# Performance work log

Hardware: AMD Instinct MI355X
Metric: run time of the kernel (lower is better)

Reference implementation:

```python
import jax, jax.numpy as jnp
import numpy as np

B, F, V, D, H = 16384, 45, 10000, 256, 32


def setup_inputs() -> dict:
    key = jax.random.key(0)
    ks = jax.random.split(key, 6)
    src = jax.random.randint(ks[0], (B, F), 0, V, dtype=jnp.int64 if jax.config.jax_enable_x64 else jnp.int32)
    tables = jax.random.normal(ks[1], (F, V, D), dtype=jnp.float32) * 0.02
    W1 = jax.random.normal(ks[2], (D, H), dtype=jnp.float32) * 0.05
    b1 = jax.random.normal(ks[3], (H,), dtype=jnp.float32) * 0.05
    W2 = jax.random.normal(ks[4], (H, 1), dtype=jnp.float32) * 0.05
    b2 = jax.random.normal(ks[5], (1,), dtype=jnp.float32) * 0.05
    return {"src": src, "tables": tables, "W1": W1, "b1": b1, "W2": W2, "b2": b2}


def reference(src, tables, W1, b1, W2, b2):
    # Fused multi-table gather: emb[b, f] = tables[f, src[b, f]]  -> [B, F, D]
    feat_idx = jnp.arange(F)[None, :]            # [1, F]
    emb = tables[feat_idx, src]                  # [B, F, D]
    # Small MLP applied per feature position, then sum over features.
    h = jnp.einsum('bfd,dh->bfh', emb, W1) + b1  # [B, F, 32]
    out = jnp.einsum('bfh,ho->bfo', h, W2) + b2  # [B, F, 1]
    return jnp.sum(out, axis=1)                  # [B, 1]
```

## Files before the change

### kernel.cpp

```cpp
#include <hip/hip_runtime.h>


#define BN 16384
#define FN 45
#define VN 10000
#define DN 256
#define HN 32

__global__ void prep_w_kernel(const float* __restrict__ W1,
                              const float* __restrict__ b1,
                              const float* __restrict__ W2,
                              const float* __restrict__ b2,
                              float* __restrict__ w_out,
                              float* __restrict__ c_out) {
    int d = threadIdx.x;
    float s = 0.f;
#pragma unroll
    for (int h = 0; h < HN; ++h) s += W1[d * HN + h] * W2[h];
    w_out[d] = s;
    if (d == 0) {
        float cc = 0.f;
#pragma unroll
        for (int h = 0; h < HN; ++h) cc += b1[h] * W2[h];
        c_out[0] = cc + b2[0];
    }
}

__global__ __launch_bounds__(256, 8)
void row_dot_kernel(const float* __restrict__ tables,
                    const float* __restrict__ w,
                    float* __restrict__ t,
                    int R) {
    const int lane = threadIdx.x & 63;
    const int wave_in_block = threadIdx.x >> 6;
    const int waves_per_block = blockDim.x >> 6;
    const int nwaves = gridDim.x * waves_per_block;
    int wave = blockIdx.x * waves_per_block + wave_in_block;

    const float4 wv = reinterpret_cast<const float4*>(w)[lane];

    for (int r = wave; r < R; r += nwaves) {
        const float4 v =
            reinterpret_cast<const float4*>(tables + (size_t)r * DN)[lane];
        float s = v.x * wv.x + v.y * wv.y + v.z * wv.z + v.w * wv.w;
#pragma unroll
        for (int m = 1; m < 64; m <<= 1) s += __shfl_xor(s, m);
        if (lane == 0) t[r] = s;
    }
}

__global__ __launch_bounds__(256)
void gather_sum_kernel(const int* __restrict__ src,
                       const float* __restrict__ t,
                       const float* __restrict__ c,
                       float* __restrict__ out) {
    const int lane = threadIdx.x & 63;
    const int wave = blockIdx.x * (blockDim.x >> 6) + (threadIdx.x >> 6);
    if (wave >= BN) return;

    float s = 0.f;
    if (lane < FN) {
        const int idx = src[wave * FN + lane];
        s = t[lane * VN + idx];
    }
#pragma unroll
    for (int m = 1; m < 64; m <<= 1) s += __shfl_xor(s, m);
    if (lane == 0) out[wave] = s + (float)FN * c[0];
}

extern "C" void kernel_launch(void* const* d_in, const int* in_sizes, int n_in,
                              void* d_out, int out_size, void* d_ws, size_t ws_size,
                              hipStream_t stream) {
    const int* src = (const int*)d_in[0];
    const float* tables = (const float*)d_in[1];
    const float* W1 = (const float*)d_in[2];
    const float* b1 = (const float*)d_in[3];
    const float* W2 = (const float*)d_in[4];
    const float* b2 = (const float*)d_in[5];
    float* out = (float*)d_out;

    float* ws = (float*)d_ws;
    float* w = ws;
    float* c = ws + 256;
    float* t = ws + 512;
    const int R = FN * VN;

    prep_w_kernel<<<1, 256, 0, stream>>>(W1, b1, W2, b2, w, c);

    row_dot_kernel<<<2048, 256, 0, stream>>>(tables, w, t, R);

    gather_sum_kernel<<<4096, 256, 0, stream>>>(src, t, c, out);
}
```

Measured before the change: 598.6 us.

## Fuse into cooperative kernel and skip table rows never referenced by src

```diff
diff --git a/kernel.cpp b/kernel.cpp
--- a/kernel.cpp
+++ b/kernel.cpp
@@ -1,4 +1,7 @@
 #include <hip/hip_runtime.h>
+#include <hip/hip_cooperative_groups.h>
+
+namespace cg = cooperative_groups;
 
 
 #define BN 16384
@@ -6,66 +9,77 @@
 #define VN 10000
 #define DN 256
 #define HN 32
+#define RN (FN * VN)
+#define NBLK 1024
+#define NTHR 256
+#define NWAVE (NBLK * 4)
+#define NTHREADS (NBLK * NTHR)
 
-__global__ void prep_w_kernel(const float* __restrict__ W1,
-                              const float* __restrict__ b1,
-                              const float* __restrict__ W2,
-                              const float* __restrict__ b2,
-                              float* __restrict__ w_out,
-                              float* __restrict__ c_out) {
-    int d = threadIdx.x;
-    float s = 0.f;
+__global__ __launch_bounds__(NTHR, 4)
+void fused_kernel(const int* __restrict__ src,
+                  const float* __restrict__ tables,
+                  const float* __restrict__ W1,
+                  const float* __restrict__ b1,
+                  const float* __restrict__ W2,
+                  const float* __restrict__ b2,
+                  float* __restrict__ out,
+                  float* __restrict__ t,
+                  unsigned char* __restrict__ flags) {
+    cg::grid_group grid = cg::this_grid();
+    const int tid = threadIdx.x;
+    const int lane = tid & 63;
+    const int wid = tid >> 6;
+    const int gwave = blockIdx.x * 4 + wid;
+    const int gtid = blockIdx.x * NTHR + tid;
+
+    __shared__ __align__(16) float w_s[DN];
+    __shared__ float c_s;
+
+    {
+        float s = 0.f;
 #pragma unroll
-    for (int h = 0; h < HN; ++h) s += W1[d * HN + h] * W2[h];
-    w_out[d] = s;
-    if (d == 0) {
-        float cc = 0.f;
+        for (int h = 0; h < HN; ++h) s += W1[tid * HN + h] * W2[h];
+        w_s[tid] = s;
+        if (tid == 0) {
+            float cc = 0.f;
 #pragma unroll
-        for (int h = 0; h < HN; ++h) cc += b1[h] * W2[h];
-        c_out[0] = cc + b2[0];
+            for (int h = 0; h < HN; ++h) cc += b1[h] * W2[h];
+            c_s = (float)FN * (cc + b2[0]);
+        }
     }
-}
+    {
+        unsigned int* fw = reinterpret_cast<unsigned int*>(flags);
+        for (int i = gtid; i < RN / 4; i += NTHREADS) fw[i] = 0u;
+    }
+    grid.sync();
 
-__global__ __launch_bounds__(256, 8)
-void row_dot_kernel(const float* __restrict__ tables,
-                    const float* __restrict__ w,
-                    float* __restrict__ t,
-                    int R) {
-    const int lane = threadIdx.x & 63;
-    const int wave_in_block = threadIdx.x >> 6;
-    const int waves_per_block = blockDim.x >> 6;
-    const int nwaves = gridDim.x * waves_per_block;
-    int wave = blockIdx.x * waves_per_block + wave_in_block;
+    for (int i = gtid; i < BN * FN; i += NTHREADS) {
+        const int f = i % FN;
+        flags[f * VN + src[i]] = (unsigned char)1;
+    }
+    grid.sync();
 
-    const float4 wv = reinterpret_cast<const float4*>(w)[lane];
+    {
+        const float4 wv = reinterpret_cast<const float4*>(w_s)[lane];
+        for (int r = gwave; r < RN; r += NWAVE) {
+            if (!flags[r]) continue;
+            const float4 v =
+                reinterpret_cast<const float4*>(tables + (size_t)r * DN)[lane];
+            float s = v.x * wv.x + v.y * wv.y + v.z * wv.z + v.w * wv.w;
+#pragma unroll
+            for (int m = 1; m < 64; m <<= 1) s += __shfl_xor(s, m);
+            if (lane == 0) t[r] = s;
+        }
+    }
+    grid.sync();
 
-    for (int r = wave; r < R; r += nwaves) {
-        const float4 v =
-            reinterpret_cast<const float4*>(tables + (size_t)r * DN)[lane];
-        float s = v.x * wv.x + v.y * wv.y + v.z * wv.z + v.w * wv.w;
+    for (int b = gwave; b < BN; b += NWAVE) {
+        float s = 0.f;
+        if (lane < FN) s = t[lane * VN + src[b * FN + lane]];
 #pragma unroll
         for (int m = 1; m < 64; m <<= 1) s += __shfl_xor(s, m);
-        if (lane == 0) t[r] = s;
+        if (lane == 0) out[b] = s + c_s;
     }
-}
-
-__global__ __launch_bounds__(256)
-void gather_sum_kernel(const int* __restrict__ src,
-                       const float* __restrict__ t,
-                       const float* __restrict__ c,
-                       float* __restrict__ out) {
-    const int lane = threadIdx.x & 63;
-    const int wave = blockIdx.x * (blockDim.x >> 6) + (threadIdx.x >> 6);
-    if (wave >= BN) return;
-
-    float s = 0.f;
-    if (lane < FN) {
-        const int idx = src[wave * FN + lane];
-        s = t[lane * VN + idx];
-    }
-#pragma unroll
-    for (int m = 1; m < 64; m <<= 1) s += __shfl_xor(s, m);
-    if (lane == 0) out[wave] = s + (float)FN * c[0];
 }
 
 extern "C" void kernel_launch(void* const* d_in, const int* in_sizes, int n_in,
@@ -79,15 +93,12 @@
     const float* b2 = (const float*)d_in[5];
     float* out = (float*)d_out;
 
-    float* ws = (float*)d_ws;
-    float* w = ws;
-    float* c = ws + 256;
-    float* t = ws + 512;
-    const int R = FN * VN;
+    float* t = (float*)d_ws;
+    unsigned char* flags = (unsigned char*)d_ws + (size_t)RN * sizeof(float);
 
-    prep_w_kernel<<<1, 256, 0, stream>>>(W1, b1, W2, b2, w, c);
-
-    row_dot_kernel<<<2048, 256, 0, stream>>>(tables, w, t, R);
-
-    gather_sum_kernel<<<4096, 256, 0, stream>>>(src, t, c, out);
+    void* args[] = {(void*)&src, (void*)&tables, (void*)&W1, (void*)&b1,
+                    (void*)&W2,  (void*)&b2,     (void*)&out, (void*)&t,
+                    (void*)&flags};
+    hipLaunchCooperativeKernel((void*)fused_kernel, dim3(NBLK), dim3(NTHR),
+                               args, 0, stream);
 }
```

After: 942.9 us. 1.58x slower.

## Compute row dots only for table rows referenced by src

Applied to the files above, without the earlier changes.

```diff
diff --git a/kernel.cpp b/kernel.cpp
--- a/kernel.cpp
+++ b/kernel.cpp
@@ -6,14 +6,15 @@
 #define VN 10000
 #define DN 256
 #define HN 32
+#define RN (FN * VN)
 
-__global__ void prep_w_kernel(const float* __restrict__ W1,
-                              const float* __restrict__ b1,
-                              const float* __restrict__ W2,
-                              const float* __restrict__ b2,
-                              float* __restrict__ w_out,
-                              float* __restrict__ c_out) {
-    int d = threadIdx.x;
+__global__ void prep_kernel(const float* __restrict__ W1,
+                            const float* __restrict__ b1,
+                            const float* __restrict__ W2,
+                            const float* __restrict__ b2,
+                            float* __restrict__ w_out,
+                            float* __restrict__ c_out) {
+    const int d = threadIdx.x;
     float s = 0.f;
 #pragma unroll
     for (int h = 0; h < HN; ++h) s += W1[d * HN + h] * W2[h];
@@ -22,50 +23,54 @@
         float cc = 0.f;
 #pragma unroll
         for (int h = 0; h < HN; ++h) cc += b1[h] * W2[h];
-        c_out[0] = cc + b2[0];
+        c_out[0] = (float)FN * (cc + b2[0]);
     }
 }
 
-__global__ __launch_bounds__(256, 8)
-void row_dot_kernel(const float* __restrict__ tables,
-                    const float* __restrict__ w,
-                    float* __restrict__ t,
-                    int R) {
-    const int lane = threadIdx.x & 63;
-    const int wave_in_block = threadIdx.x >> 6;
-    const int waves_per_block = blockDim.x >> 6;
-    const int nwaves = gridDim.x * waves_per_block;
-    int wave = blockIdx.x * waves_per_block + wave_in_block;
-
-    const float4 wv = reinterpret_cast<const float4*>(w)[lane];
-
-    for (int r = wave; r < R; r += nwaves) {
-        const float4 v =
-            reinterpret_cast<const float4*>(tables + (size_t)r * DN)[lane];
-        float s = v.x * wv.x + v.y * wv.y + v.z * wv.z + v.w * wv.w;
-#pragma unroll
-        for (int m = 1; m < 64; m <<= 1) s += __shfl_xor(s, m);
-        if (lane == 0) t[r] = s;
-    }
+__global__ void scatter_kernel(const int* __restrict__ src,
+                               unsigned char* __restrict__ flags) {
+    const int i = blockIdx.x * blockDim.x + threadIdx.x;
+    const int f = i % FN;
+    flags[f * VN + src[i]] = (unsigned char)1;
 }
 
-__global__ __launch_bounds__(256)
-void gather_sum_kernel(const int* __restrict__ src,
-                       const float* __restrict__ t,
-                       const float* __restrict__ c,
-                       float* __restrict__ out) {
-    const int lane = threadIdx.x & 63;
-    const int wave = blockIdx.x * (blockDim.x >> 6) + (threadIdx.x >> 6);
-    if (wave >= BN) return;
+__global__ void row_dot_kernel(const float* __restrict__ tables,
+                               const float* __restrict__ w_glob,
+                               const unsigned char* __restrict__ flags,
+                               float* __restrict__ t) {
+    __shared__ __align__(16) float w_s[DN];
+    w_s[threadIdx.x] = w_glob[threadIdx.x];
+    __syncthreads();
 
+    const int r = blockIdx.x * blockDim.x + threadIdx.x;
+    if (r >= RN) return;
+    if (!flags[r]) return;
+
+    const float4* __restrict__ row =
+        reinterpret_cast<const float4*>(tables + (size_t)r * DN);
+    const float4* __restrict__ wv4 = reinterpret_cast<const float4*>(w_s);
     float s = 0.f;
-    if (lane < FN) {
-        const int idx = src[wave * FN + lane];
-        s = t[lane * VN + idx];
+#pragma unroll
+    for (int j = 0; j < DN / 4; ++j) {
+        const float4 v = row[j];
+        const float4 wv = wv4[j];
+        s += v.x * wv.x + v.y * wv.y + v.z * wv.z + v.w * wv.w;
     }
+    t[r] = s;
+}
+
+__global__ void gather_kernel(const int* __restrict__ src,
+                              const float* __restrict__ t,
+                              const float* __restrict__ c,
+                              float* __restrict__ out) {
+    const int b = blockIdx.x * blockDim.x + threadIdx.x;
+    const int* __restrict__ s_row = src + (size_t)b * FN;
+    float s = 0.f;
 #pragma unroll
-    for (int m = 1; m < 64; m <<= 1) s += __shfl_xor(s, m);
-    if (lane == 0) out[wave] = s + (float)FN * c[0];
+    for (int f = 0; f < FN; ++f) {
+        s += t[f * VN + s_row[f]];
+    }
+    out[b] = s + c[0];
 }
 
 extern "C" void kernel_launch(void* const* d_in, const int* in_sizes, int n_in,
@@ -79,15 +84,14 @@
     const float* b2 = (const float*)d_in[5];
     float* out = (float*)d_out;
 
-    float* ws = (float*)d_ws;
-    float* w = ws;
-    float* c = ws + 256;
-    float* t = ws + 512;
-    const int R = FN * VN;
+    float* t = (float*)d_ws;
+    float* w = t + RN;
+    float* c = w + DN;
+    unsigned char* flags = (unsigned char*)(c + 1);
 
-    prep_w_kernel<<<1, 256, 0, stream>>>(W1, b1, W2, b2, w, c);
-
-    row_dot_kernel<<<2048, 256, 0, stream>>>(tables, w, t, R);
-
-    gather_sum_kernel<<<4096, 256, 0, stream>>>(src, t, c, out);
+    prep_kernel<<<1, 256, 0, stream>>>(W1, b1, W2, b2, w, c);
+    hipMemsetAsync(flags, 0, RN, stream);
+    scatter_kernel<<<(BN * FN) / 256, 256, 0, stream>>>(src, flags);
+    row_dot_kernel<<<(RN + 255) / 256, 256, 0, stream>>>(tables, w, flags, t);
+    gather_kernel<<<BN / 256, 256, 0, stream>>>(src, t, c, out);
 }
```

Measured after the change: 630.8 us. +5.4%, slower.
